# Optimization experiments

Measured on AMD Instinct MI355X. Metric: run time of the kernel, lower is better.

## Reference

```python
import jax, jax.numpy as jnp
import numpy as np

B, H, W, C = 2, 64, 64, 256
G, K, L = 16, 9, 2
Cg = C // G


def _ln(x, g, b, eps=1e-6):
    m = jnp.mean(x, -1, keepdims=True)
    v = jnp.mean((x - m) ** 2, -1, keepdims=True)
    return (x - m) * jax.lax.rsqrt(v + eps) * g + b


def _conv(x, w, b=None, groups=1):
    y = jax.lax.conv_general_dilated(x, w, (1, 1), 'SAME',
        dimension_numbers=('NHWC', 'HWIO', 'NHWC'), feature_group_count=groups)
    return y if b is None else y + b


def _gelu(x):
    return jax.nn.gelu(x, approximate=False)  # torch nn.GELU (exact erf)


def _dcnv3(x, dw_w, dw_b, dwn_g, dwn_b, off_w, off_b, msk_w, msk_b,
           inp_w, inp_b, out_w, out_b, offset_scale=1.0):
    # x: [B,H,W,C] channels-last. kernel=3, stride=1, pad=1, dilation=1.
    xp = x @ inp_w + inp_b                                   # input_proj
    f = _gelu(_ln(_conv(x, dw_w, dw_b, groups=C), dwn_g, dwn_b))  # dw_conv branch
    off = (f @ off_w + off_b).reshape(B, H, W, G, K, 2) * offset_scale  # pixel units (x,y)
    mask = jax.nn.softmax((f @ msk_w + msk_b).reshape(B, H, W, G, K), axis=-1)
    dy, dx = jnp.meshgrid(jnp.arange(3.0) - 1.0, jnp.arange(3.0) - 1.0, indexing='ij')
    gx = dx.reshape(-1)
    gy = dy.reshape(-1)  # [K] kernel dilation grid
    # sampling locations in the zero-padded (pad=1) frame; pixel i center = i+0.5
    loc_x = (jnp.arange(W, dtype=x.dtype) + 1.5)[None, None, :, None, None] + gx + off[..., 0]
    loc_y = (jnp.arange(H, dtype=x.dtype) + 1.5)[None, :, None, None, None] + gy + off[..., 1]
    xg = jnp.pad(xp, ((0, 0), (1, 1), (1, 1), (0, 0))).reshape(B, H + 2, W + 2, G, Cg)
    px = loc_x - 0.5
    py = loc_y - 0.5
    x0 = jnp.floor(px).astype(jnp.int32)
    y0 = jnp.floor(py).astype(jnp.int32)
    fx = (px - x0)[..., None]
    fy = (py - y0)[..., None]
    Hp, Wp = H + 2, W + 2
    bi = jnp.arange(B).reshape(B, 1, 1, 1, 1)
    gi = jnp.arange(G).reshape(1, 1, 1, G, 1)

    def gather(yi, xi):  # zero padding outside bounds (grid_sample padding_mode='zeros')
        ok = ((yi >= 0) & (yi < Hp) & (xi >= 0) & (xi < Wp)).astype(x.dtype)[..., None]
        return xg[bi, jnp.clip(yi, 0, Hp - 1), jnp.clip(xi, 0, Wp - 1), gi] * ok

    top = gather(y0, x0) * (1 - fx) + gather(y0, x0 + 1) * fx
    bot = gather(y0 + 1, x0) * (1 - fx) + gather(y0 + 1, x0 + 1) * fx
    samp = top * (1 - fy) + bot * fy                         # [B,H,W,G,K,Cg]
    out = (samp * mask[..., None]).sum(4).reshape(B, H, W, C)
    return out @ out_w + out_b                               # output_proj


def _leffn(x, dc_w, dc_b, g, b, c1_w, c1_b, c2_w, c2_b, gamma):
    y = _ln(_conv(x, dc_w, dc_b, groups=C), g, b)
    y = _gelu(y @ c1_w + c1_b) @ c2_w + c2_b
    return x + gamma * y


def _cbam(x, w1, w2, sa_w, g, b):
    fc = lambda v: jax.nn.relu(v @ w1) @ w2
    ca = jax.nn.sigmoid(fc(x.mean((1, 2))) + fc(x.max((1, 2))))[:, None, None, :]
    x = x * ca
    sm = jnp.stack([x.mean(-1), x.max(-1)], -1)              # [B,H,W,2]
    x = x * jax.nn.sigmoid(_conv(sm, sa_w))
    return _ln(x, g, b)


def _upsample(x, w, bb, g, bt):
    y = jax.image.resize(x, (B, 2 * H, 2 * W, C), 'bilinear')  # align_corners=False
    y = _conv(y, w, bb)                                        # 3x3, C -> C//2
    return _gelu(_ln(y, g, bt))


def _forward(x, ln1_g, ln1_b, dw_w, dw_b, dwn_g, dwn_b, off_w, off_b, msk_w, msk_b,
             inp_w, inp_b, out_w, out_b, ln2_g, ln2_b, dc_w, dc_b, fn_g, fn_b,
             c1_w, c1_b, c2_w, c2_b, ffn_gamma, ca_w1, ca_w2, sa_w, cb_g, cb_b,
             nf_g, nf_b, up_w, up_b, up_g, up_bt):
    x = _cbam(x, ca_w1, ca_w2, sa_w, cb_g, cb_b)
    for i in range(L):  # fixed small depth; structural loop
        x = x + _dcnv3(_ln(x, ln1_g[i], ln1_b[i]), dw_w[i], dw_b[i], dwn_g[i], dwn_b[i],
                       off_w[i], off_b[i], msk_w[i], msk_b[i], inp_w[i], inp_b[i],
                       out_w[i], out_b[i])
        x = x + _leffn(_ln(x, ln2_g[i], ln2_b[i]), dc_w[i], dc_b[i], fn_g[i], fn_b[i],
                       c1_w[i], c1_b[i], c2_w[i], c2_b[i], ffn_gamma[i])
    x = _ln(x, nf_g, nf_b)
    return _upsample(x, up_w, up_b, up_g, up_bt)


def setup_inputs() -> dict:
    ks = iter(jax.random.split(jax.random.key(0), 80))
    r = lambda shp, s=0.02: jax.random.normal(next(ks), shp, dtype=jnp.float32) * s
    one = lambda shp: jnp.ones(shp, jnp.float32)
    zero = lambda shp: jnp.zeros(shp, jnp.float32)
    return dict(
        x=jax.random.normal(next(ks), (B, H, W, C), dtype=jnp.float32),
        ln1_g=one((L, C)), ln1_b=zero((L, C)),
        dw_w=r((L, 3, 3, 1, C)), dw_b=zero((L, C)),
        dwn_g=one((L, C)), dwn_b=zero((L, C)),
        off_w=r((L, C, G * K * 2), 0.01), off_b=zero((L, G * K * 2)),
        msk_w=r((L, C, G * K)), msk_b=zero((L, G * K)),
        inp_w=r((L, C, C)), inp_b=zero((L, C)),
        out_w=r((L, C, C)), out_b=zero((L, C)),
        ln2_g=one((L, C)), ln2_b=zero((L, C)),
        dc_w=r((L, 7, 7, 1, C)), dc_b=zero((L, C)),
        fn_g=one((L, C)), fn_b=zero((L, C)),
        c1_w=r((L, C, 4 * C)), c1_b=zero((L, 4 * C)),
        c2_w=r((L, 4 * C, C)), c2_b=zero((L, C)),
        ffn_gamma=0.7 * one((L, C)),
        ca_w1=r((C, C // 16)), ca_w2=r((C // 16, C)),
        sa_w=r((7, 7, 2, 1)),
        cb_g=one((C,)), cb_b=zero((C,)),
        nf_g=one((C,)), nf_b=zero((C,)),
        up_w=r((3, 3, C, C // 2)), up_b=zero((C // 2,)),
        up_g=one((C // 2,)), up_bt=zero((C // 2,)),
    )


def reference(x, ln1_g, ln1_b, dw_w, dw_b, dwn_g, dwn_b, off_w, off_b, msk_w, msk_b,
              inp_w, inp_b, out_w, out_b, ln2_g, ln2_b, dc_w, dc_b, fn_g, fn_b,
              c1_w, c1_b, c2_w, c2_b, ffn_gamma, ca_w1, ca_w2, sa_w, cb_g, cb_b,
              nf_g, nf_b, up_w, up_b, up_g, up_bt):
    return _forward(x, ln1_g, ln1_b, dw_w, dw_b, dwn_g, dwn_b, off_w, off_b, msk_w, msk_b,
                    inp_w, inp_b, out_w, out_b, ln2_g, ln2_b, dc_w, dc_b, fn_g, fn_b,
                    c1_w, c1_b, c2_w, c2_b, ffn_gamma, ca_w1, ca_w2, sa_w, cb_g, cb_b,
                    nf_g, nf_b, up_w, up_b, up_g, up_bt)
```

## Files before the change

kernel.cpp:

```cpp
#include <hip/hip_runtime.h>
#include <math.h>

#define B_ 2
#define H_ 64
#define W_ 64
#define C_ 256
#define G_ 16
#define HW_ (H_*W_)
#define M_ (B_*HW_)
#define C4_ (4*C_)
#define OFFN_ 288
#define MSKN_ 144
#define OMN_ 432
#define UH_ 128
#define UW_ 128
#define MUP_ (B_*UH_*UW_)
#define KUP_ (9*C_)
#define NOUT_ 128

typedef short short8 __attribute__((ext_vector_type(8)));
typedef float f32x4 __attribute__((ext_vector_type(4)));
typedef unsigned short us4 __attribute__((ext_vector_type(4)));

__device__ __forceinline__ float gelu_f(float x){
  return 0.5f * x * (1.f + erff(x * 0.70710678118654752440f));
}
__device__ __forceinline__ float sigmoid_f(float x){ return 1.f/(1.f+expf(-x)); }
__device__ __forceinline__ unsigned short f2bf(float x){
  unsigned int u = __float_as_uint(x);
  unsigned int r = (u + 0x7fffu + ((u>>16)&1u)) >> 16;
  return (unsigned short)r;
}
__device__ __forceinline__ float bf2f(unsigned short u){
  return __uint_as_float(((unsigned int)u) << 16);
}
__device__ __forceinline__ float bfl(unsigned int u){ return __uint_as_float(u<<16); }
__device__ __forceinline__ float bfh(unsigned int u){ return __uint_as_float(u & 0xffff0000u); }
__device__ __forceinline__ unsigned int pk(float a, float b){
  return (unsigned int)f2bf(a) | ((unsigned int)f2bf(b) << 16);
}

__device__ __forceinline__ void block_sum2(float& s, float& ss, float* sm){
  #pragma unroll
  for (int off=32; off>0; off>>=1){ s += __shfl_down(s, off); ss += __shfl_down(ss, off); }
  int lane = threadIdx.x & 63, wid = threadIdx.x >> 6;
  if (lane == 0){ sm[wid] = s; sm[4+wid] = ss; }
  __syncthreads();
  float a = 0.f, b = 0.f;
  int nw = blockDim.x >> 6;
  for (int i=0;i<nw;i++){ a += sm[i]; b += sm[4+i]; }
  s = a; ss = b;
}

__device__ __forceinline__ void block_summax(float& s, float& m, float* sm){
  #pragma unroll
  for (int off=32; off>0; off>>=1){ s += __shfl_down(s, off); m = fmaxf(m, __shfl_down(m, off)); }
  int lane = threadIdx.x & 63, wid = threadIdx.x >> 6;
  if (lane == 0){ sm[wid] = s; sm[4+wid] = m; }
  __syncthreads();
  float a = 0.f, b = -3.4e38f;
  int nw = blockDim.x >> 6;
  for (int i=0;i<nw;i++){ a += sm[i]; b = fmaxf(b, sm[4+i]); }
  s = a; m = b;
}

#define NJOBS 13
struct WtJobs {
  const float* src[NJOBS];
  unsigned short* dst[NJOBS];
  int Kd[NJOBS], Nd[NJOBS];
  int tOff[NJOBS+1];
};

__global__ __launch_bounds__(256) void k_wt_pool(WtJobs J, const float* __restrict__ Xin,
    float* __restrict__ psum, float* __restrict__ pmax){
  __shared__ float tile[32][33];
  int bid = blockIdx.x;
  int nwt = J.tOff[NJOBS];
  if (bid >= nwt){
    int lb = bid - nwt;
    int chunk = lb & 127, b = lb >> 7; int c = threadIdx.x;
    const float* p = Xin + (((size_t)b*HW_) + chunk*32)*C_ + c;
    float s = 0.f, m = -3.4e38f;
    for (int i=0;i<32;i++){ float v = p[(size_t)i*C_]; s += v; m = fmaxf(m, v); }
    psum[(b*128+chunk)*C_+c] = s; pmax[(b*128+chunk)*C_+c] = m;
    return;
  }
  int j = 0;
  while (bid >= J.tOff[j+1]) j++;
  int lt = bid - J.tOff[j];
  const float* W = J.src[j];
  unsigned short* Wt = J.dst[j];
  int Kd = J.Kd[j], Nd = J.Nd[j];
  int ktiles = Kd >> 5;
  int k0 = (lt % ktiles) * 32, n0 = (lt / ktiles) * 32;
  int t = threadIdx.x;
  int r = t>>3, c4 = (t&7)*4;
  float4 v = make_float4(0.f,0.f,0.f,0.f);
  if (n0 + c4 < Nd) v = *(const float4*)(W + (size_t)(k0+r)*Nd + n0 + c4);
  tile[c4+0][r]=v.x; tile[c4+1][r]=v.y; tile[c4+2][r]=v.z; tile[c4+3][r]=v.w;
  __syncthreads();
  if (n0 + r < Nd){
    us4 o;
    o.x = f2bf(tile[r][c4+0]); o.y = f2bf(tile[r][c4+1]);
    o.z = f2bf(tile[r][c4+2]); o.w = f2bf(tile[r][c4+3]);
    *(us4*)(Wt + (size_t)(n0+r)*Kd + k0 + c4) = o;
  }
}

__global__ __launch_bounds__(512) void k_ca(const float* __restrict__ psum, const float* __restrict__ pmax,
    const float* __restrict__ w1, const float* __restrict__ w2, float* __restrict__ ca){
  __shared__ float pm[2][256], px[2][256], hh[2][2][16];
  int t = threadIdx.x;
  {
    int b = t >> 8, c = t & 255;
    float s = 0.f, m = -3.4e38f;
    for (int ch=0; ch<128; ch++){ s += psum[(b*128+ch)*256+c]; m = fmaxf(m, pmax[(b*128+ch)*256+c]); }
    pm[b][c] = s * (1.f/4096.f); px[b][c] = m;
  }
  __syncthreads();
  if (t < 64){
    int b = t >> 5, typ = (t >> 4) & 1, j = t & 15;
    const float* src = typ ? px[b] : pm[b];
    float a = 0.f;
    for (int c2=0;c2<256;c2++) a += src[c2]*w1[c2*16+j];
    hh[b][typ][j] = fmaxf(a, 0.f);
  }
  __syncthreads();
  {
    int b = t >> 8, c = t & 255;
    float a = 0.f;
    for (int j=0;j<16;j++) a += (hh[b][0][j]+hh[b][1][j]) * w2[j*256+c];
    ca[b*256+c] = sigmoid_f(a);
  }
}

__global__ __launch_bounds__(256) void k_apply_ca(const float* __restrict__ Xin, float* __restrict__ X,
    const float* __restrict__ ca, float* __restrict__ smean, float* __restrict__ smax){
  __shared__ float sm[12];
  int pix = blockIdx.x, c = threadIdx.x;
  int b = pix >> 12;
  float v = Xin[(size_t)pix*C_+c] * ca[b*C_+c];
  X[(size_t)pix*C_+c] = v;
  float s = v, m = v;
  block_summax(s, m, sm);
  if (c == 0){ smean[pix] = s * (1.f/C_); smax[pix] = m; }
}

__global__ __launch_bounds__(256) void k_sa_mul_ln_ln1(float* __restrict__ X,
    const float* __restrict__ smean, const float* __restrict__ smax, const float* __restrict__ wsa,
    const float* __restrict__ g, const float* __restrict__ b,
    const float* __restrict__ g1, const float* __restrict__ b1, unsigned short* __restrict__ Tb){
  __shared__ float sm[12];
  __shared__ float sav;
  int pix = blockIdx.x, c = threadIdx.x;
  int bb2 = pix >> 12, hw = pix & 4095, h = hw >> 6, ww = hw & 63;
  {
    float s = 0.f;
    if (c < 49){
      int ky = c / 7, kx = c % 7;
      int hh = h + ky - 3, xx = ww + kx - 3;
      if (hh >= 0 && hh < H_ && xx >= 0 && xx < W_){
        int q = (bb2<<12) + (hh<<6) + xx;
        s = smean[q]*wsa[c*2+0] + smax[q]*wsa[c*2+1];
      }
    }
    if (c < 64){
      #pragma unroll
      for (int off=32; off>0; off>>=1) s += __shfl_down(s, off);
      if (c == 0) sav = sigmoid_f(s);
    }
  }
  __syncthreads();
  float v = X[(size_t)pix*C_+c] * sav;
  float s = v, ss = v*v;
  block_sum2(s, ss, sm);
  float mean = s * (1.f/C_), var = ss*(1.f/C_) - mean*mean;
  float r = rsqrtf(var + 1e-6f);
  float x0 = (v-mean)*r*g[c] + b[c];
  X[(size_t)pix*C_+c] = x0;
  __syncthreads();
  s = x0; ss = x0*x0;
  block_sum2(s, ss, sm);
  mean = s * (1.f/C_); var = ss*(1.f/C_) - mean*mean;
  r = rsqrtf(var + 1e-6f);
  Tb[(size_t)pix*C_+c] = f2bf((x0-mean)*r*g1[c] + b1[c]);
}

template<int KS, int DOGELU>
__device__ __forceinline__ void dwconv_body(int t, const unsigned short* __restrict__ T,
    unsigned short* __restrict__ Out,
    const float* __restrict__ w, const float* __restrict__ bias,
    const float* __restrict__ g, const float* __restrict__ bb){
  constexpr int R = KS/2;
  int pix = t >> 5, grp = t & 31;
  int c0 = grp*8;
  int b = pix >> 12, hw = pix & 4095, h = hw >> 6, ww = hw & 63;
  float acc[8];
  {
    float4 b0 = *(const float4*)(bias + c0), b1 = *(const float4*)(bias + c0 + 4);
    acc[0]=b0.x; acc[1]=b0.y; acc[2]=b0.z; acc[3]=b0.w;
    acc[4]=b1.x; acc[5]=b1.y; acc[6]=b1.z; acc[7]=b1.w;
  }
  const unsigned short* tb = T + ((size_t)b*HW_)*C_ + c0;
  for (int ky=0;ky<KS;ky++){
    int hh = h + ky - R; if (hh < 0 || hh >= H_) continue;
    for (int kx=0;kx<KS;kx++){
      int xx = ww + kx - R; if (xx < 0 || xx >= W_) continue;
      uint4 a = *(const uint4*)(tb + ((size_t)hh*W_+xx)*C_);
      const float* wp = w + (ky*KS+kx)*C_ + c0;
      float4 w0 = *(const float4*)wp, w1 = *(const float4*)(wp+4);
      acc[0] += bfl(a.x)*w0.x; acc[1] += bfh(a.x)*w0.y;
      acc[2] += bfl(a.y)*w0.z; acc[3] += bfh(a.y)*w0.w;
      acc[4] += bfl(a.z)*w1.x; acc[5] += bfh(a.z)*w1.y;
      acc[6] += bfl(a.w)*w1.z; acc[7] += bfh(a.w)*w1.w;
    }
  }
  float s = 0.f, ss = 0.f;
  #pragma unroll
  for (int i=0;i<8;i++){ s += acc[i]; ss += acc[i]*acc[i]; }
  #pragma unroll
  for (int off=1; off<32; off<<=1){ s += __shfl_xor(s, off); ss += __shfl_xor(ss, off); }
  float mean = s * (1.f/C_), var = ss*(1.f/C_) - mean*mean;
  float r = rsqrtf(var + 1e-6f);
  float4 g0 = *(const float4*)(g + c0), g1 = *(const float4*)(g + c0 + 4);
  float4 p0 = *(const float4*)(bb + c0), p1 = *(const float4*)(bb + c0 + 4);
  float o[8];
  o[0]=(acc[0]-mean)*r*g0.x+p0.x; o[1]=(acc[1]-mean)*r*g0.y+p0.y;
  o[2]=(acc[2]-mean)*r*g0.z+p0.z; o[3]=(acc[3]-mean)*r*g0.w+p0.w;
  o[4]=(acc[4]-mean)*r*g1.x+p1.x; o[5]=(acc[5]-mean)*r*g1.y+p1.y;
  o[6]=(acc[6]-mean)*r*g1.z+p1.z; o[7]=(acc[7]-mean)*r*g1.w+p1.w;
  if (DOGELU){
    #pragma unroll
    for (int i=0;i<8;i++) o[i] = gelu_f(o[i]);
  }
  uint4 ov;
  ov.x = pk(o[0],o[1]); ov.y = pk(o[2],o[3]); ov.z = pk(o[4],o[5]); ov.w = pk(o[6],o[7]);
  *(uint4*)(Out + (size_t)pix*C_ + c0) = ov;
}

__global__ __launch_bounds__(256) void k_dw7(const unsigned short* __restrict__ T,
    unsigned short* __restrict__ Out,
    const float* __restrict__ w, const float* __restrict__ bias,
    const float* __restrict__ g, const float* __restrict__ bb){
  dwconv_body<7,0>(blockIdx.x*256 + threadIdx.x, T, Out, w, bias, g, bb);
}

__global__ __launch_bounds__(256) void k_inp_dw3(
    const unsigned short* __restrict__ Tb, const unsigned short* __restrict__ Bt,
    unsigned short* __restrict__ XPb, const float* __restrict__ inpb,
    unsigned short* __restrict__ Fb,
    const float* __restrict__ dww, const float* __restrict__ dwb,
    const float* __restrict__ dwng, const float* __restrict__ dwnb)
{
  constexpr int LD = 40;
  __shared__ unsigned short As[64*LD];
  __shared__ unsigned short Bs[128*LD];
  const int bid = blockIdx.x;
  const int tid = threadIdx.x;
  if (bid >= 256){
    dwconv_body<3,1>((bid-256)*256 + tid, Tb, Fb, dww, dwb, dwng, dwnb);
    return;
  }
  const int wave = tid >> 6, lane = tid & 63;
  const int m0 = (bid & 127) * 64, n0 = (bid >> 7) * 128;
  const int wm0 = (wave >> 1) * 32;
  const int wn0 = (wave & 1) * 64;
  f32x4 acc[2][4] = {};
  const int lm = lane & 15, kq = lane >> 4;

  for (int k0 = 0; k0 < C_; k0 += 32){
    {
      int r = tid >> 2, cc = (tid & 3) << 3;
      short8 v = *(const short8*)(Tb + (size_t)(m0 + r)*C_ + k0 + cc);
      *(short8*)(As + r*LD + cc) = v;
    }
    #pragma unroll
    for (int i=0;i<2;i++){
      int ch = tid + 256*i;
      int r = ch >> 2, cc = (ch & 3) << 3;
      short8 v = *(const short8*)(Bt + (size_t)(n0 + r)*C_ + k0 + cc);
      *(short8*)(Bs + r*LD + cc) = v;
    }
    __syncthreads();
    short8 af[2], bf[4];
    #pragma unroll
    for (int mi=0;mi<2;mi++) af[mi] = *(const short8*)(As + (wm0 + mi*16 + lm)*LD + kq*8);
    #pragma unroll
    for (int ni=0;ni<4;ni++)  bf[ni] = *(const short8*)(Bs + (wn0 + ni*16 + lm)*LD + kq*8);
    #pragma unroll
    for (int mi=0;mi<2;mi++)
      #pragma unroll
      for (int ni=0;ni<4;ni++)
        acc[mi][ni] = __builtin_amdgcn_mfma_f32_16x16x32_bf16(af[mi], bf[ni], acc[mi][ni], 0,0,0);
    __syncthreads();
  }
  #pragma unroll
  for (int mi=0;mi<2;mi++){
    #pragma unroll
    for (int ni=0;ni<4;ni++){
      int n = n0 + wn0 + ni*16 + lm;
      float bv = inpb[n];
      #pragma unroll
      for (int r=0;r<4;r++){
        int m = m0 + wm0 + mi*16 + kq*4 + r;
        XPb[(size_t)m*C_ + n] = f2bf(acc[mi][ni][r] + bv);
      }
    }
  }
}

template<int TM, int EP, int OUTBF>
__global__ __launch_bounds__(256) void k_gemm_mfma(
    const unsigned short* __restrict__ A, const unsigned short* __restrict__ Bt,
    void* __restrict__ OutV, const float* __restrict__ bias,
    const float* __restrict__ bias2, int Ni, int Ki)
{
  constexpr int LD = 40;
  __shared__ unsigned short As[TM*LD];
  __shared__ unsigned short Bs[128*LD];
  const int tid = threadIdx.x;
  const int wave = tid >> 6, lane = tid & 63;
  const int m0 = blockIdx.x * TM, n0 = blockIdx.y * 128;
  const int wm0 = (wave >> 1) * (TM/2);
  const int wn0 = (wave & 1) * 64;
  constexpr int MI = (TM+31)/32;
  f32x4 acc[MI][4] = {};
  const int lm = lane & 15, kq = lane >> 4;

  for (int k0 = 0; k0 < Ki; k0 += 32){
    for (int ch = tid; ch < TM*4; ch += 256){
      int r = ch >> 2, cc = (ch & 3) << 3;
      short8 v = *(const short8*)(A + (size_t)(m0 + r)*Ki + k0 + cc);
      *(short8*)(As + r*LD + cc) = v;
    }
    #pragma unroll
    for (int i=0;i<2;i++){
      int ch = tid + 256*i;
      int r = ch >> 2, cc = (ch & 3) << 3;
      short8 v = {};
      if (n0 + r < Ni) v = *(const short8*)(Bt + (size_t)(n0 + r)*Ki + k0 + cc);
      *(short8*)(Bs + r*LD + cc) = v;
    }
    __syncthreads();
    short8 af[MI], bf[4];
    #pragma unroll
    for (int mi=0;mi<MI;mi++) af[mi] = *(const short8*)(As + (wm0 + mi*16 + lm)*LD + kq*8);
    #pragma unroll
    for (int ni=0;ni<4;ni++)  bf[ni] = *(const short8*)(Bs + (wn0 + ni*16 + lm)*LD + kq*8);
    #pragma unroll
    for (int mi=0;mi<MI;mi++)
      #pragma unroll
      for (int ni=0;ni<4;ni++)
        acc[mi][ni] = __builtin_amdgcn_mfma_f32_16x16x32_bf16(af[mi], bf[ni], acc[mi][ni], 0,0,0);
    __syncthreads();
  }
  #pragma unroll
  for (int mi=0;mi<MI;mi++){
    #pragma unroll
    for (int ni=0;ni<4;ni++){
      int n = n0 + wn0 + ni*16 + lm;
      if (n < Ni){
        float bv;
        if constexpr (EP==4) bv = (n < OFFN_) ? bias[n] : bias2[n-OFFN_];
        else bv = bias[n];
        #pragma unroll
        for (int r=0;r<4;r++){
          int m = m0 + wm0 + mi*16 + kq*4 + r;
          size_t o = (size_t)m*Ni + n;
          float v = acc[mi][ni][r] + bv;
          if constexpr (EP==1) v = gelu_f(v);
          if constexpr (OUTBF) ((unsigned short*)OutV)[o] = f2bf(v);
          else                 ((float*)OutV)[o] = v;
        }
      }
    }
  }
}

template<int EP>
__global__ __launch_bounds__(256) void k_gemm_ln(
    const unsigned short* __restrict__ A, const unsigned short* __restrict__ Bt,
    float* __restrict__ X, const float* __restrict__ bias,
    const unsigned short* __restrict__ res2b, const float* __restrict__ gamma,
    unsigned short* __restrict__ OutTb,
    const float* __restrict__ lng, const float* __restrict__ lnb, int Ki)
{
  constexpr int LD = 40;
  __shared__ unsigned short As[32*LD];
  __shared__ unsigned short Bs[256*LD];
  __shared__ float rs[32][2], rq[32][2];
  const int tid = threadIdx.x;
  const int wave = tid >> 6, lane = tid & 63;
  const int m0 = blockIdx.x * 32;
  const int wm0 = (wave >> 1) * 16;
  const int wn0 = (wave & 1) * 128;
  const int lm = lane & 15, kq = lane >> 4;
  f32x4 acc[8] = {};

  for (int k0 = 0; k0 < Ki; k0 += 32){
    if (tid < 128){
      int r = tid >> 2, cc = (tid & 3) << 3;
      short8 v = *(const short8*)(A + (size_t)(m0 + r)*Ki + k0 + cc);
      *(short8*)(As + r*LD + cc) = v;
    }
    #pragma unroll
    for (int i=0;i<4;i++){
      int ch = tid + 256*i;
      int r = ch >> 2, cc = (ch & 3) << 3;
      short8 v = *(const short8*)(Bt + (size_t)r*Ki + k0 + cc);
      *(short8*)(Bs + r*LD + cc) = v;
    }
    __syncthreads();
    short8 af = *(const short8*)(As + (wm0 + lm)*LD + kq*8);
    short8 bf[8];
    #pragma unroll
    for (int ni=0;ni<8;ni++) bf[ni] = *(const short8*)(Bs + (wn0 + ni*16 + lm)*LD + kq*8);
    #pragma unroll
    for (int ni=0;ni<8;ni++)
      acc[ni] = __builtin_amdgcn_mfma_f32_16x16x32_bf16(af, bf[ni], acc[ni], 0,0,0);
    __syncthreads();
  }
  int nn[8]; float bv[8], gv[8];
  #pragma unroll
  for (int ni=0;ni<8;ni++){
    nn[ni] = wn0 + ni*16 + lm;
    bv[ni] = bias[nn[ni]];
    if constexpr (EP==3) gv[ni] = gamma[nn[ni]];
  }
  float ps[4] = {}, pq[4] = {};
  #pragma unroll
  for (int r=0;r<4;r++){
    int m = m0 + wm0 + kq*4 + r;
    #pragma unroll
    for (int ni=0;ni<8;ni++){
      size_t o = (size_t)m*C_ + nn[ni];
      float v = acc[ni][r] + bv[ni];
      if constexpr (EP==2) v = X[o] + v;
      if constexpr (EP==3) v = X[o] + bf2f(res2b[o]) + gv[ni]*v;
      X[o] = v;
      acc[ni][r] = v;
      ps[r] += v; pq[r] += v*v;
    }
  }
  #pragma unroll
  for (int off=1; off<16; off<<=1){
    #pragma unroll
    for (int r=0;r<4;r++){ ps[r] += __shfl_xor(ps[r], off); pq[r] += __shfl_xor(pq[r], off); }
  }
  if (lm == 0){
    #pragma unroll
    for (int r=0;r<4;r++){
      rs[wm0 + kq*4 + r][wave & 1] = ps[r];
      rq[wm0 + kq*4 + r][wave & 1] = pq[r];
    }
  }
  __syncthreads();
  float lg[8], lb[8];
  #pragma unroll
  for (int ni=0;ni<8;ni++){ lg[ni] = lng[nn[ni]]; lb[ni] = lnb[nn[ni]]; }
  #pragma unroll
  for (int r=0;r<4;r++){
    int row = wm0 + kq*4 + r;
    int m = m0 + row;
    float s = rs[row][0] + rs[row][1];
    float q = rq[row][0] + rq[row][1];
    float mean = s * (1.f/C_), var = q*(1.f/C_) - mean*mean;
    float rstd = rsqrtf(var + 1e-6f);
    #pragma unroll
    for (int ni=0;ni<8;ni++){
      size_t o = (size_t)m*C_ + nn[ni];
      OutTb[o] = f2bf((acc[ni][r]-mean)*rstd*lg[ni] + lb[ni]);
    }
  }
}

__global__ __launch_bounds__(256) void k_dcn(const unsigned short* __restrict__ xp,
    const float* __restrict__ OM, unsigned short* __restrict__ S){
  __shared__ float lom[16*OMN_];
  int pix0 = blockIdx.x * 16;
  {
    const float* gsrc = OM + (size_t)pix0*OMN_;
    for (int idx = threadIdx.x; idx < 16*OMN_; idx += 256) lom[idx] = gsrc[idx];
  }
  __syncthreads();
  int pl = threadIdx.x >> 4, g = threadIdx.x & 15;
  int pix = pix0 + pl;
  int b = pix >> 12, hw = pix & 4095, h = hw >> 6, ww = hw & 63;
  const float* offp = lom + pl*OMN_ + g*18;
  const float* mp   = lom + pl*OMN_ + OFFN_ + g*9;
  const unsigned short* xpb = xp + ((size_t)b*HW_)*C_ + g*16;
  float e[9]; float mx = -3.4e38f;
  #pragma unroll
  for (int k=0;k<9;k++){ e[k] = mp[k]; mx = fmaxf(mx, e[k]); }
  float ssum = 0.f;
  #pragma unroll
  for (int k=0;k<9;k++){ e[k] = expf(e[k]-mx); ssum += e[k]; }
  float rinv = 1.f/ssum;
  float acc[16] = {};
  #pragma unroll
  for (int k=0;k<9;k++){
    float ox = offp[k*2+0], oy = offp[k*2+1];
    float px = (float)(ww + (k%3)) + ox;
    float py = (float)(h  + (k/3)) + oy;
    int x0 = (int)floorf(px), y0 = (int)floorf(py);
    float fx = px - (float)x0, fy = py - (float)y0;
    float mk = e[k]*rinv;
    float w00 = mk*(1.f-fx)*(1.f-fy), w01 = mk*fx*(1.f-fy);
    float w10 = mk*(1.f-fx)*fy,       w11 = mk*fx*fy;
    #define CORNER(yy,xx,WGT) do{ \
      if ((yy)>=1 && (yy)<=H_ && (xx)>=1 && (xx)<=W_){ \
        const unsigned short* p = xpb + ((size_t)((yy)-1)*W_ + ((xx)-1))*C_; \
        uint4 a0 = *(const uint4*)p; uint4 a1 = *(const uint4*)(p+8); \
        acc[0]+=WGT*bfl(a0.x); acc[1]+=WGT*bfh(a0.x); acc[2]+=WGT*bfl(a0.y); acc[3]+=WGT*bfh(a0.y); \
        acc[4]+=WGT*bfl(a0.z); acc[5]+=WGT*bfh(a0.z); acc[6]+=WGT*bfl(a0.w); acc[7]+=WGT*bfh(a0.w); \
        acc[8]+=WGT*bfl(a1.x); acc[9]+=WGT*bfh(a1.x); acc[10]+=WGT*bfl(a1.y); acc[11]+=WGT*bfh(a1.y); \
        acc[12]+=WGT*bfl(a1.z); acc[13]+=WGT*bfh(a1.z); acc[14]+=WGT*bfl(a1.w); acc[15]+=WGT*bfh(a1.w); \
      } \
    }while(0)
    CORNER(y0,   x0,   w00);
    CORNER(y0,   x0+1, w01);
    CORNER(y0+1, x0,   w10);
    CORNER(y0+1, x0+1, w11);
    #undef CORNER
  }
  unsigned short* sp = S + (size_t)pix*C_ + g*16;
  uint4 o0, o1;
  o0.x = pk(acc[0],acc[1]);   o0.y = pk(acc[2],acc[3]);
  o0.z = pk(acc[4],acc[5]);   o0.w = pk(acc[6],acc[7]);
  o1.x = pk(acc[8],acc[9]);   o1.y = pk(acc[10],acc[11]);
  o1.z = pk(acc[12],acc[13]); o1.w = pk(acc[14],acc[15]);
  *(uint4*)sp = o0;
  *(uint4*)(sp+8) = o1;
}

__global__ __launch_bounds__(256) void k_upsample(const unsigned short* __restrict__ T, unsigned short* __restrict__ U){
  int t = blockIdx.x*256 + threadIdx.x;
  int opix = t >> 5, grp = t & 31;
  int c0 = grp*8;
  int ox = opix & 127, oy = (opix >> 7) & 127, b = opix >> 14;
  float sy = oy*0.5f - 0.25f, sx = ox*0.5f - 0.25f;
  int y0 = (int)floorf(sy), x0 = (int)floorf(sx);
  float fy = sy - (float)y0, fx = sx - (float)x0;
  int y0c = min(max(y0,0),H_-1), y1c = min(max(y0+1,0),H_-1);
  int x0c = min(max(x0,0),W_-1), x1c = min(max(x0+1,0),W_-1);
  const unsigned short* tb = T + ((size_t)b*HW_)*C_ + c0;
  uint4 q00 = *(const uint4*)(tb + ((size_t)y0c*W_+x0c)*C_);
  uint4 q01 = *(const uint4*)(tb + ((size_t)y0c*W_+x1c)*C_);
  uint4 q10 = *(const uint4*)(tb + ((size_t)y1c*W_+x0c)*C_);
  uint4 q11 = *(const uint4*)(tb + ((size_t)y1c*W_+x1c)*C_);
  float w00=(1.f-fy)*(1.f-fx), w01=(1.f-fy)*fx, w10=fy*(1.f-fx), w11=fy*fx;
  float o[8];
  o[0]=w00*bfl(q00.x)+w01*bfl(q01.x)+w10*bfl(q10.x)+w11*bfl(q11.x);
  o[1]=w00*bfh(q00.x)+w01*bfh(q01.x)+w10*bfh(q10.x)+w11*bfh(q11.x);
  o[2]=w00*bfl(q00.y)+w01*bfl(q01.y)+w10*bfl(q10.y)+w11*bfl(q11.y);
  o[3]=w00*bfh(q00.y)+w01*bfh(q01.y)+w10*bfh(q10.y)+w11*bfh(q11.y);
  o[4]=w00*bfl(q00.z)+w01*bfl(q01.z)+w10*bfl(q10.z)+w11*bfl(q11.z);
  o[5]=w00*bfh(q00.z)+w01*bfh(q01.z)+w10*bfh(q10.z)+w11*bfh(q11.z);
  o[6]=w00*bfl(q00.w)+w01*bfl(q01.w)+w10*bfl(q10.w)+w11*bfl(q11.w);
  o[7]=w00*bfh(q00.w)+w01*bfh(q01.w)+w10*bfh(q10.w)+w11*bfh(q11.w);
  uint4 ov;
  ov.x = pk(o[0],o[1]); ov.y = pk(o[2],o[3]); ov.z = pk(o[4],o[5]); ov.w = pk(o[6],o[7]);
  *(uint4*)(U + (size_t)opix*C_ + c0) = ov;
}

__global__ __launch_bounds__(256) void k_upconv_ln(
    const unsigned short* __restrict__ U, const unsigned short* __restrict__ Wt,
    float* __restrict__ Out, const float* __restrict__ bias,
    const float* __restrict__ g, const float* __restrict__ bb)
{
  constexpr int LD = 136;
  __shared__ unsigned short As[64*LD];
  __shared__ unsigned short Bs[128*LD];
  __shared__ float rs[64][2], rq[64][2];
  const int tid = threadIdx.x;
  const int wave = tid >> 6, lane = tid & 63;
  const int m0 = blockIdx.x * 64;
  const int wm0 = (wave >> 1) * 32;
  const int wn0 = (wave & 1) * 64;
  const int lm = lane & 15, kq = lane >> 4;
  f32x4 acc[2][4] = {};
  const int r0 = tid >> 2, cA0 = (tid & 3) << 5;
  const int ma = m0 + r0;
  const int ba = ma >> 14, oya = (ma >> 7) & 127, oxa = ma & 127;

  for (int k0 = 0; k0 < KUP_; k0 += 128){
    int tap = k0 >> 8, cc0 = k0 & 255;
    int dy = tap/3 - 1, dx = tap%3 - 1;
    {
      int iy = oya + dy, ix = oxa + dx;
      bool ok = (iy >= 0 && iy < UH_ && ix >= 0 && ix < UW_);
      const unsigned short* src = U + (((size_t)ba*UH_ + iy)*UW_ + ix)*C_ + cc0 + cA0;
      #pragma unroll
      for (int i=0;i<4;i++){
        short8 v = {};
        if (ok) v = *(const short8*)(src + i*8);
        *(short8*)(As + r0*LD + cA0 + i*8) = v;
      }
    }
    #pragma unroll
    for (int i=0;i<8;i++){
      int ch = tid + 256*i;
      int r = ch >> 4, cc = (ch & 15) << 3;
      short8 v = *(const short8*)(Wt + (size_t)r*KUP_ + k0 + cc);
      *(short8*)(Bs + r*LD + cc) = v;
    }
    __syncthreads();
    short8 af[2][4], bf4[4][4];
    #pragma unroll
    for (int mi=0;mi<2;mi++)
      #pragma unroll
      for (int kk=0;kk<4;kk++)
        af[mi][kk] = *(const short8*)(As + (wm0 + mi*16 + lm)*LD + kk*32 + kq*8);
    #pragma unroll
    for (int ni=0;ni<4;ni++)
      #pragma unroll
      for (int kk=0;kk<4;kk++)
        bf4[ni][kk] = *(const short8*)(Bs + (wn0 + ni*16 + lm)*LD + kk*32 + kq*8);
    #pragma unroll
    for (int kk=0;kk<4;kk++)
      #pragma unroll
      for (int mi=0;mi<2;mi++)
        #pragma unroll
        for (int ni=0;ni<4;ni++)
          acc[mi][ni] = __builtin_amdgcn_mfma_f32_16x16x32_bf16(af[mi][kk], bf4[ni][kk], acc[mi][ni], 0,0,0);
    __syncthreads();
  }
  int nn[4]; float bv[4];
  #pragma unroll
  for (int ni=0;ni<4;ni++){ nn[ni] = wn0 + ni*16 + lm; bv[ni] = bias[nn[ni]]; }
  float ps[2][4] = {}, pq[2][4] = {};
  #pragma unroll
  for (int mi=0;mi<2;mi++)
    #pragma unroll
    for (int r=0;r<4;r++)
      #pragma unroll
      for (int ni=0;ni<4;ni++){
        float v = acc[mi][ni][r] + bv[ni];
        acc[mi][ni][r] = v;
        ps[mi][r] += v; pq[mi][r] += v*v;
      }
  #pragma unroll
  for (int off=1; off<16; off<<=1){
    #pragma unroll
    for (int mi=0;mi<2;mi++)
      #pragma unroll
      for (int r=0;r<4;r++){ ps[mi][r] += __shfl_xor(ps[mi][r], off); pq[mi][r] += __shfl_xor(pq[mi][r], off); }
  }
  if (lm == 0){
    #pragma unroll
    for (int mi=0;mi<2;mi++)
      #pragma unroll
      for (int r=0;r<4;r++){
        rs[wm0 + mi*16 + kq*4 + r][wave & 1] = ps[mi][r];
        rq[wm0 + mi*16 + kq*4 + r][wave & 1] = pq[mi][r];
      }
  }
  __syncthreads();
  float gv[4], pv[4];
  #pragma unroll
  for (int ni=0;ni<4;ni++){ gv[ni] = g[nn[ni]]; pv[ni] = bb[nn[ni]]; }
  #pragma unroll
  for (int mi=0;mi<2;mi++)
    #pragma unroll
    for (int r=0;r<4;r++){
      int row = wm0 + mi*16 + kq*4 + r;
      int m = m0 + row;
      float s = rs[row][0] + rs[row][1];
      float q = rq[row][0] + rq[row][1];
      float mean = s * (1.f/NOUT_), var = q*(1.f/NOUT_) - mean*mean;
      float rstd = rsqrtf(var + 1e-6f);
      #pragma unroll
      for (int ni=0;ni<4;ni++)
        Out[(size_t)m*NOUT_ + nn[ni]] = gelu_f((acc[mi][ni][r]-mean)*rstd*gv[ni] + pv[ni]);
    }
}

extern "C" void kernel_launch(void* const* d_in, const int* in_sizes, int n_in,
                              void* d_out, int out_size, void* d_ws, size_t ws_size,
                              hipStream_t stream)
{
  (void)in_sizes; (void)n_in; (void)out_size; (void)ws_size;
  const float* x_in = (const float*)d_in[0];
  char* w = (char*)d_ws;
  const size_t MB = 1u<<20;
  float* X    = (float*)(w + 0*MB);
  float* OM   = (float*)(w + 8*MB);
  unsigned short* MIDb = (unsigned short*)(w + 22*MB);
  unsigned short* Ub   = MIDb;
  unsigned short* Tb   = (unsigned short*)(w + 38*MB);
  unsigned short* Fb   = (unsigned short*)(w + 42*MB);
  unsigned short* XPb  = (unsigned short*)(w + 46*MB);
  unsigned short* DW7b = (unsigned short*)(w + 50*MB);
  unsigned short* Sb   = (unsigned short*)(w + 54*MB);
  unsigned short* WT   = (unsigned short*)(w + 58*MB);
  float* psum = (float*)(w + 62*MB);
  float* pmax = psum + 65536;
  float* ca   = pmax + 65536;
  float* smean= ca + 512;
  float* smax = smean + 8192;

  unsigned short* WtInp[2], *WtOut[2], *WtOM[2], *WtC1[2], *WtC2[2];
  {
    size_t o = 0;
    for (int i=0;i<2;i++){
      WtInp[i] = WT + o; o += 65536;
      WtOut[i] = WT + o; o += 65536;
      WtOM[i]  = WT + o; o += 110592;
      WtC1[i]  = WT + o; o += 262144;
      WtC2[i]  = WT + o; o += 262144;
    }
  }
  unsigned short* WtUp = WT + 1531904;

  WtJobs J;
  int toff = 0;
  {
    int ji = 0;
    auto add = [&](const float* s, unsigned short* d, int Kd, int Nd){
      J.src[ji]=s; J.dst[ji]=d; J.Kd[ji]=Kd; J.Nd[ji]=Nd;
      J.tOff[ji]=toff; toff += (Kd>>5) * ((Nd+31)>>5); ji++;
    };
    for (int i=0;i<2;i++){
      add((const float*)d_in[11] + (size_t)i*C_*C_,   WtInp[i], C_, C_);
      add((const float*)d_in[13] + (size_t)i*C_*C_,   WtOut[i], C_, C_);
      add((const float*)d_in[7]  + (size_t)i*C_*OFFN_, WtOM[i], C_, OFFN_);
      add((const float*)d_in[9]  + (size_t)i*C_*MSKN_, WtOM[i] + (size_t)OFFN_*C_, C_, MSKN_);
      add((const float*)d_in[21] + (size_t)i*C_*C4_,  WtC1[i], C_, C4_);
      add((const float*)d_in[23] + (size_t)i*C4_*C_,  WtC2[i], C4_, C_);
    }
    add((const float*)d_in[33], WtUp, KUP_, NOUT_);
    J.tOff[ji] = toff;
  }
  k_wt_pool<<<toff + 256,256,0,stream>>>(J, x_in, psum, pmax);

  k_ca<<<1,512,0,stream>>>(psum, pmax, (const float*)d_in[26], (const float*)d_in[27], ca);
  k_apply_ca<<<M_,256,0,stream>>>(x_in, X, ca, smean, smax);
  k_sa_mul_ln_ln1<<<M_,256,0,stream>>>(X, smean, smax, (const float*)d_in[28],
      (const float*)d_in[29], (const float*)d_in[30],
      (const float*)d_in[1], (const float*)d_in[2], Tb);

  for (int i=0;i<2;i++){
    const float* dww  = (const float*)d_in[3] + i*9*C_;
    const float* dwb  = (const float*)d_in[4] + i*C_;
    const float* dwng = (const float*)d_in[5] + i*C_;
    const float* dwnb = (const float*)d_in[6] + i*C_;
    const float* offb = (const float*)d_in[8] + i*OFFN_;
    const float* mskb = (const float*)d_in[10] + i*MSKN_;
    const float* inpb = (const float*)d_in[12] + i*C_;
    const float* outb = (const float*)d_in[14] + i*C_;
    const float* ln2g = (const float*)d_in[15] + i*C_;
    const float* ln2b = (const float*)d_in[16] + i*C_;
    const float* dcw  = (const float*)d_in[17] + i*49*C_;
    const float* dcb  = (const float*)d_in[18] + i*C_;
    const float* fng  = (const float*)d_in[19] + i*C_;
    const float* fnb  = (const float*)d_in[20] + i*C_;
    const float* c1b  = (const float*)d_in[22] + i*C4_;
    const float* c2b  = (const float*)d_in[24] + i*C_;
    const float* gam  = (const float*)d_in[25] + i*C_;
    const float* nxg = (i==0) ? (const float*)d_in[1] + C_ : (const float*)d_in[31];
    const float* nxb = (i==0) ? (const float*)d_in[2] + C_ : (const float*)d_in[32];

    k_inp_dw3<<<256 + M_*32/256,256,0,stream>>>(Tb, WtInp[i], XPb, inpb, Fb, dww, dwb, dwng, dwnb);
    k_gemm_mfma<64,4,0><<<dim3(M_/64,4),256,0,stream>>>(Fb, WtOM[i], OM, offb, mskb, OMN_, C_);
    k_dcn<<<M_/16,256,0,stream>>>(XPb, OM, Sb);
    k_gemm_ln<2><<<M_/32,256,0,stream>>>(Sb, WtOut[i], X, outb, nullptr, nullptr, Tb, ln2g, ln2b, C_);

    k_dw7<<<M_*32/256,256,0,stream>>>(Tb, DW7b, dcw, dcb, fng, fnb);
    k_gemm_mfma<128,1,1><<<dim3(M_/128,8),256,0,stream>>>(DW7b, WtC1[i], MIDb, c1b, nullptr, C4_, C_);
    k_gemm_ln<3><<<M_/32,256,0,stream>>>(MIDb, WtC2[i], X, c2b, Tb, gam, Tb, nxg, nxb, C4_);
  }

  k_upsample<<<MUP_*32/256,256,0,stream>>>(Tb, Ub);
  k_upconv_ln<<<MUP_/64,256,0,stream>>>(Ub, WtUp, (float*)d_out, (const float*)d_in[34],
      (const float*)d_in[35], (const float*)d_in[36]);
}
```

Baseline: 502.6 us.

## Fuse deformable sampling into output-projection GEMM with residual LayerNorm

The DCNv3 bilinear sampling kernel now writes its 32-pixel tile of sampled features directly into shared memory, and the same block then runs the output-projection MFMA GEMM, residual add and LayerNorm. This removes the intermediate S buffer round-trip through global memory and one kernel launch per layer. In exchange, offsets and masks are read from global memory directly instead of being staged in LDS, and the per-block gather work doubles while the grid shrinks, which may change latency hiding.

```diff
diff --git a/kernel.cpp b/kernel.cpp
--- a/kernel.cpp
+++ b/kernel.cpp
@@ -475,63 +475,143 @@
   }
 }
 
-__global__ __launch_bounds__(256) void k_dcn(const unsigned short* __restrict__ xp,
-    const float* __restrict__ OM, unsigned short* __restrict__ S){
-  __shared__ float lom[16*OMN_];
-  int pix0 = blockIdx.x * 16;
-  {
-    const float* gsrc = OM + (size_t)pix0*OMN_;
-    for (int idx = threadIdx.x; idx < 16*OMN_; idx += 256) lom[idx] = gsrc[idx];
-  }
-  __syncthreads();
-  int pl = threadIdx.x >> 4, g = threadIdx.x & 15;
-  int pix = pix0 + pl;
-  int b = pix >> 12, hw = pix & 4095, h = hw >> 6, ww = hw & 63;
-  const float* offp = lom + pl*OMN_ + g*18;
-  const float* mp   = lom + pl*OMN_ + OFFN_ + g*9;
-  const unsigned short* xpb = xp + ((size_t)b*HW_)*C_ + g*16;
-  float e[9]; float mx = -3.4e38f;
-  #pragma unroll
-  for (int k=0;k<9;k++){ e[k] = mp[k]; mx = fmaxf(mx, e[k]); }
-  float ssum = 0.f;
-  #pragma unroll
-  for (int k=0;k<9;k++){ e[k] = expf(e[k]-mx); ssum += e[k]; }
-  float rinv = 1.f/ssum;
-  float acc[16] = {};
-  #pragma unroll
-  for (int k=0;k<9;k++){
-    float ox = offp[k*2+0], oy = offp[k*2+1];
-    float px = (float)(ww + (k%3)) + ox;
-    float py = (float)(h  + (k/3)) + oy;
-    int x0 = (int)floorf(px), y0 = (int)floorf(py);
-    float fx = px - (float)x0, fy = py - (float)y0;
-    float mk = e[k]*rinv;
-    float w00 = mk*(1.f-fx)*(1.f-fy), w01 = mk*fx*(1.f-fy);
-    float w10 = mk*(1.f-fx)*fy,       w11 = mk*fx*fy;
-    #define CORNER(yy,xx,WGT) do{ \
-      if ((yy)>=1 && (yy)<=H_ && (xx)>=1 && (xx)<=W_){ \
-        const unsigned short* p = xpb + ((size_t)((yy)-1)*W_ + ((xx)-1))*C_; \
-        uint4 a0 = *(const uint4*)p; uint4 a1 = *(const uint4*)(p+8); \
-        acc[0]+=WGT*bfl(a0.x); acc[1]+=WGT*bfh(a0.x); acc[2]+=WGT*bfl(a0.y); acc[3]+=WGT*bfh(a0.y); \
-        acc[4]+=WGT*bfl(a0.z); acc[5]+=WGT*bfh(a0.z); acc[6]+=WGT*bfl(a0.w); acc[7]+=WGT*bfh(a0.w); \
-        acc[8]+=WGT*bfl(a1.x); acc[9]+=WGT*bfh(a1.x); acc[10]+=WGT*bfl(a1.y); acc[11]+=WGT*bfh(a1.y); \
-        acc[12]+=WGT*bfl(a1.z); acc[13]+=WGT*bfh(a1.z); acc[14]+=WGT*bfl(a1.w); acc[15]+=WGT*bfh(a1.w); \
-      } \
-    }while(0)
-    CORNER(y0,   x0,   w00);
-    CORNER(y0,   x0+1, w01);
-    CORNER(y0+1, x0,   w10);
-    CORNER(y0+1, x0+1, w11);
-    #undef CORNER
-  }
-  unsigned short* sp = S + (size_t)pix*C_ + g*16;
-  uint4 o0, o1;
-  o0.x = pk(acc[0],acc[1]);   o0.y = pk(acc[2],acc[3]);
-  o0.z = pk(acc[4],acc[5]);   o0.w = pk(acc[6],acc[7]);
-  o1.x = pk(acc[8],acc[9]);   o1.y = pk(acc[10],acc[11]);
-  o1.z = pk(acc[12],acc[13]); o1.w = pk(acc[14],acc[15]);
-  *(uint4*)sp = o0;
-  *(uint4*)(sp+8) = o1;
+__global__ __launch_bounds__(256) void k_dcn_gemm_ln(
+    const unsigned short* __restrict__ xp, const float* __restrict__ OM,
+    const unsigned short* __restrict__ Bt,
+    float* __restrict__ X, const float* __restrict__ bias,
+    unsigned short* __restrict__ OutTb,
+    const float* __restrict__ lng, const float* __restrict__ lnb)
+{
+  constexpr int LDA = 264;
+  constexpr int LD = 40;
+  __shared__ unsigned short As[32*LDA];
+  __shared__ unsigned short Bs[256*LD];
+  __shared__ float rs[32][2], rq[32][2];
+  const int tid = threadIdx.x;
+  const int wave = tid >> 6, lane = tid & 63;
+  const int m0 = blockIdx.x * 32;
+  const int wm0 = (wave >> 1) * 16;
+  const int wn0 = (wave & 1) * 128;
+  const int lm = lane & 15, kq = lane >> 4;
+
+  #pragma unroll
+  for (int it=0; it<2; it++){
+    int task = tid + 256*it;
+    int pl = task >> 4, g = task & 15;
+    int pix = m0 + pl;
+    int b = pix >> 12, hw = pix & 4095, h = hw >> 6, ww = hw & 63;
+    const float* offp = OM + (size_t)pix*OMN_ + g*18;
+    const float* mp   = OM + (size_t)pix*OMN_ + OFFN_ + g*9;
+    const unsigned short* xpb = xp + ((size_t)b*HW_)*C_ + g*16;
+    float e[9]; float mx = -3.4e38f;
+    #pragma unroll
+    for (int k=0;k<9;k++){ e[k] = mp[k]; mx = fmaxf(mx, e[k]); }
+    float ssum = 0.f;
+    #pragma unroll
+    for (int k=0;k<9;k++){ e[k] = expf(e[k]-mx); ssum += e[k]; }
+    float rinv = 1.f/ssum;
+    float acc[16] = {};
+    #pragma unroll
+    for (int k=0;k<9;k++){
+      float ox = offp[k*2+0], oy = offp[k*2+1];
+      float px = (float)(ww + (k%3)) + ox;
+      float py = (float)(h  + (k/3)) + oy;
+      int x0 = (int)floorf(px), y0 = (int)floorf(py);
+      float fx = px - (float)x0, fy = py - (float)y0;
+      float mk = e[k]*rinv;
+      float w00 = mk*(1.f-fx)*(1.f-fy), w01 = mk*fx*(1.f-fy);
+      float w10 = mk*(1.f-fx)*fy,       w11 = mk*fx*fy;
+      #define CORNER(yy,xx,WGT) do{ \
+        if ((yy)>=1 && (yy)<=H_ && (xx)>=1 && (xx)<=W_){ \
+          const unsigned short* p = xpb + ((size_t)((yy)-1)*W_ + ((xx)-1))*C_; \
+          uint4 a0 = *(const uint4*)p; uint4 a1 = *(const uint4*)(p+8); \
+          acc[0]+=WGT*bfl(a0.x); acc[1]+=WGT*bfh(a0.x); acc[2]+=WGT*bfl(a0.y); acc[3]+=WGT*bfh(a0.y); \
+          acc[4]+=WGT*bfl(a0.z); acc[5]+=WGT*bfh(a0.z); acc[6]+=WGT*bfl(a0.w); acc[7]+=WGT*bfh(a0.w); \
+          acc[8]+=WGT*bfl(a1.x); acc[9]+=WGT*bfh(a1.x); acc[10]+=WGT*bfl(a1.y); acc[11]+=WGT*bfh(a1.y); \
+          acc[12]+=WGT*bfl(a1.z); acc[13]+=WGT*bfh(a1.z); acc[14]+=WGT*bfl(a1.w); acc[15]+=WGT*bfh(a1.w); \
+        } \
+      }while(0)
+      CORNER(y0,   x0,   w00);
+      CORNER(y0,   x0+1, w01);
+      CORNER(y0+1, x0,   w10);
+      CORNER(y0+1, x0+1, w11);
+      #undef CORNER
+    }
+    uint4 o0, o1;
+    o0.x = pk(acc[0],acc[1]);   o0.y = pk(acc[2],acc[3]);
+    o0.z = pk(acc[4],acc[5]);   o0.w = pk(acc[6],acc[7]);
+    o1.x = pk(acc[8],acc[9]);   o1.y = pk(acc[10],acc[11]);
+    o1.z = pk(acc[12],acc[13]); o1.w = pk(acc[14],acc[15]);
+    *(uint4*)(As + pl*LDA + g*16) = o0;
+    *(uint4*)(As + pl*LDA + g*16 + 8) = o1;
+  }
+  __syncthreads();
+
+  f32x4 acc[8] = {};
+  for (int k0 = 0; k0 < C_; k0 += 32){
+    #pragma unroll
+    for (int i=0;i<4;i++){
+      int ch = tid + 256*i;
+      int r = ch >> 2, cc = (ch & 3) << 3;
+      short8 v = *(const short8*)(Bt + (size_t)r*C_ + k0 + cc);
+      *(short8*)(Bs + r*LD + cc) = v;
+    }
+    __syncthreads();
+    short8 af = *(const short8*)(As + (wm0 + lm)*LDA + k0 + kq*8);
+    short8 bf[8];
+    #pragma unroll
+    for (int ni=0;ni<8;ni++) bf[ni] = *(const short8*)(Bs + (wn0 + ni*16 + lm)*LD + kq*8);
+    #pragma unroll
+    for (int ni=0;ni<8;ni++)
+      acc[ni] = __builtin_amdgcn_mfma_f32_16x16x32_bf16(af, bf[ni], acc[ni], 0,0,0);
+    __syncthreads();
+  }
+  int nn[8]; float bv[8];
+  #pragma unroll
+  for (int ni=0;ni<8;ni++){ nn[ni] = wn0 + ni*16 + lm; bv[ni] = bias[nn[ni]]; }
+  float ps[4] = {}, pq[4] = {};
+  #pragma unroll
+  for (int r=0;r<4;r++){
+    int m = m0 + wm0 + kq*4 + r;
+    #pragma unroll
+    for (int ni=0;ni<8;ni++){
+      size_t o = (size_t)m*C_ + nn[ni];
+      float v = X[o] + acc[ni][r] + bv[ni];
+      X[o] = v;
+      acc[ni][r] = v;
+      ps[r] += v; pq[r] += v*v;
+    }
+  }
+  #pragma unroll
+  for (int off=1; off<16; off<<=1){
+    #pragma unroll
+    for (int r=0;r<4;r++){ ps[r] += __shfl_xor(ps[r], off); pq[r] += __shfl_xor(pq[r], off); }
+  }
+  if (lm == 0){
+    #pragma unroll
+    for (int r=0;r<4;r++){
+      rs[wm0 + kq*4 + r][wave & 1] = ps[r];
+      rq[wm0 + kq*4 + r][wave & 1] = pq[r];
+    }
+  }
+  __syncthreads();
+  float lg[8], lb[8];
+  #pragma unroll
+  for (int ni=0;ni<8;ni++){ lg[ni] = lng[nn[ni]]; lb[ni] = lnb[nn[ni]]; }
+  #pragma unroll
+  for (int r=0;r<4;r++){
+    int row = wm0 + kq*4 + r;
+    int m = m0 + row;
+    float s = rs[row][0] + rs[row][1];
+    float q = rq[row][0] + rq[row][1];
+    float mean = s * (1.f/C_), var = q*(1.f/C_) - mean*mean;
+    float rstd = rsqrtf(var + 1e-6f);
+    #pragma unroll
+    for (int ni=0;ni<8;ni++){
+      size_t o = (size_t)m*C_ + nn[ni];
+      OutTb[o] = f2bf((acc[ni][r]-mean)*rstd*lg[ni] + lb[ni]);
+    }
+  }
 }
 
 __global__ __launch_bounds__(256) void k_upsample(const unsigned short* __restrict__ T, unsigned short* __restrict__ U){
@@ -692,7 +772,6 @@
   unsigned short* Fb   = (unsigned short*)(w + 42*MB);
   unsigned short* XPb  = (unsigned short*)(w + 46*MB);
   unsigned short* DW7b = (unsigned short*)(w + 50*MB);
-  unsigned short* Sb   = (unsigned short*)(w + 54*MB);
   unsigned short* WT   = (unsigned short*)(w + 58*MB);
   float* psum = (float*)(w + 62*MB);
   float* pmax = psum + 65536;
@@ -763,8 +842,7 @@
 
     k_inp_dw3<<<256 + M_*32/256,256,0,stream>>>(Tb, WtInp[i], XPb, inpb, Fb, dww, dwb, dwng, dwnb);
     k_gemm_mfma<64,4,0><<<dim3(M_/64,4),256,0,stream>>>(Fb, WtOM[i], OM, offb, mskb, OMN_, C_);
-    k_dcn<<<M_/16,256,0,stream>>>(XPb, OM, Sb);
-    k_gemm_ln<2><<<M_/32,256,0,stream>>>(Sb, WtOut[i], X, outb, nullptr, nullptr, Tb, ln2g, ln2b, C_);
+    k_dcn_gemm_ln<<<M_/32,256,0,stream>>>(XPb, OM, WtOut[i], X, outb, Tb, ln2g, ln2b);
 
     k_dw7<<<M_*32/256,256,0,stream>>>(Tb, DW7b, dcw, dcb, fng, fnb);
     k_gemm_mfma<128,1,1><<<dim3(M_/128,8),256,0,stream>>>(DW7b, WtC1[i], MIDb, c1b, nullptr, C4_, C_);
```

After: 501.8 us. Within noise of the previous version (-0.1%).
